# Performance work log

Measured on AMD Instinct MI355X. Metric: run time of the kernel, lower is better.

Reference implementation:

```python
import jax, jax.numpy as jnp
import numpy as np

B, N, L, D = 16, 8192, 512, 384  # batch, points, latents, model dim
FF = 4 * D  # feedforward inner dim (after GEGLU split)


def _ln(x, g, b, eps=1e-5):
    m = jnp.mean(x, axis=-1, keepdims=True)
    v = jnp.mean((x - m) ** 2, axis=-1, keepdims=True)
    return (x - m) * jax.lax.rsqrt(v + eps) * g + b


def setup_inputs() -> dict:
    key = jax.random.key(0)
    ks = jax.random.split(key, 16)
    s = 0.02
    def w(k, shape):
        return jax.random.normal(k, shape, jnp.float32) * s
    return {
        "x": jax.random.normal(ks[0], (B, N, 3), jnp.float32),
        # MLP: in(3)->D, D->D, D->D, D->D with ReLU between (eqx-style depth=3)
        "mlp_w0": w(ks[1], (3, D)), "mlp_b0": jnp.zeros((D,), jnp.float32),
        "mlp_w1": w(ks[2], (D, D)), "mlp_b1": jnp.zeros((D,), jnp.float32),
        "mlp_w2": w(ks[3], (D, D)), "mlp_b2": jnp.zeros((D,), jnp.float32),
        "mlp_w3": w(ks[4], (D, D)), "mlp_b3": jnp.zeros((D,), jnp.float32),
        "query": jax.random.normal(ks[5], (1, L, D), jnp.float32),
        "ln_q_g": jnp.ones((D,), jnp.float32), "ln_q_b": jnp.zeros((D,), jnp.float32),
        "ln_ctx_g": jnp.ones((D,), jnp.float32), "ln_ctx_b": jnp.zeros((D,), jnp.float32),
        "wq": w(ks[6], (D, D)),
        "wkv": w(ks[7], (D, 2 * D)),
        "wo": w(ks[8], (D, D)), "bo": jnp.zeros((D,), jnp.float32),
        "ln_ff_g": jnp.ones((D,), jnp.float32), "ln_ff_b": jnp.zeros((D,), jnp.float32),
        "ff_w1": w(ks[9], (D, 2 * FF)), "ff_b1": jnp.zeros((2 * FF,), jnp.float32),
        "ff_w2": w(ks[10], (FF, D)), "ff_b2": jnp.zeros((D,), jnp.float32),
    }


def reference(x, mlp_w0, mlp_b0, mlp_w1, mlp_b1, mlp_w2, mlp_b2, mlp_w3, mlp_b3,
              query, ln_q_g, ln_q_b, ln_ctx_g, ln_ctx_b, wq, wkv, wo, bo,
              ln_ff_g, ln_ff_b, ff_w1, ff_b1, ff_w2, ff_b2):
    # point MLP: 3 -> D
    h = jax.nn.relu(x @ mlp_w0 + mlp_b0)
    h = jax.nn.relu(h @ mlp_w1 + mlp_b1)
    h = jax.nn.relu(h @ mlp_w2 + mlp_b2)
    ctx = h @ mlp_w3 + mlp_b3                      # [B, N, D]

    lq = jnp.broadcast_to(query, (x.shape[0], L, D))  # learnable latents

    # PreNorm cross-attention (heads=1, dim_head=D)
    qn = _ln(lq, ln_q_g, ln_q_b)
    cn = _ln(ctx, ln_ctx_g, ln_ctx_b)
    q = qn @ wq                                    # [B, L, D]
    kv = cn @ wkv
    k, v = jnp.split(kv, 2, axis=-1)               # [B, N, D] each
    scale = D ** -0.5
    sim = jnp.einsum('bid,bjd->bij', q, k) * scale # [B, L, N]
    attn = jax.nn.softmax(sim, axis=-1)
    out = jnp.einsum('bij,bjd->bid', attn, v)      # [B, L, D]
    x1 = (out @ wo + bo) + lq                      # residual

    # PreNorm GEGLU feedforward
    f = _ln(x1, ln_ff_g, ln_ff_b)
    f = f @ ff_w1 + ff_b1                          # [B, L, 2*FF]
    a, g = jnp.split(f, 2, axis=-1)
    f = a * jax.nn.gelu(g, approximate=False)      # GEGLU (exact gelu, torch default)
    return (f @ ff_w2 + ff_b2) + x1                # [B, L, D]
```

## Files before the change

kernel.cpp:

```cpp
#include <hip/hip_runtime.h>
#include <math.h>


typedef unsigned short u16;
typedef unsigned int   u32;
typedef __bf16 bf16_t;
typedef bf16_t bf16x8 __attribute__((ext_vector_type(8)));
typedef float  floatx4 __attribute__((ext_vector_type(4)));

__device__ __forceinline__ float b2f(u16 v) {
    return __uint_as_float(((u32)v) << 16);
}
__device__ __forceinline__ u16 f2b(float f) {
    bf16_t h = (bf16_t)f;
    return __builtin_bit_cast(u16, h);
}
__device__ __forceinline__ void stb4(u16* p, float4 f) {
    uint2 v;
    v.x = (u32)f2b(f.x) | ((u32)f2b(f.y) << 16);
    v.y = (u32)f2b(f.z) | ((u32)f2b(f.w) << 16);
    *(uint2*)p = v;
}

__device__ __forceinline__ void gl2lds16(u16* lds, const u16* g) {
    __builtin_amdgcn_global_load_lds(
        (const __attribute__((address_space(1))) void*)g,
        (__attribute__((address_space(3))) void*)lds, 16, 0, 0);
}

__device__ __forceinline__ void xcd_remap(int& bx, int& by, int& bz) {
    int gx = gridDim.x, gy = gridDim.y, gz = gridDim.z;
    int nb = gx * gy * gz;
    int p = bx + gx * (by + gy * bz);
    if ((nb & 7) == 0) {
        int chunk = nb >> 3;
        p = (p & 7) * chunk + (p >> 3);
    }
    bx = p % gx;
    int t = p / gx;
    by = t % gy;
    bz = t / gy;
}

__device__ __forceinline__ void xcd_remap_yf(int& bx, int& by, int& bz) {
    int gx = gridDim.x, gy = gridDim.y, gz = gridDim.z;
    int nb = gx * gy * gz;
    int p = by + gy * (bx + gx * bz);
    if ((nb & 7) == 0) {
        int chunk = nb >> 3;
        p = (p & 7) * chunk + (p >> 3);
    }
    by = p % gy;
    int t = p / gy;
    bx = t % gx;
    bz = t / gx;
}

__global__ __launch_bounds__(256) void wconv_all(
    const float* __restrict__ w1, const float* __restrict__ w2,
    const float* __restrict__ w3, const float* __restrict__ wq,
    const float* __restrict__ wkv, const float* __restrict__ wo,
    const float* __restrict__ ffw1, const float* __restrict__ ffw2,
    u16* __restrict__ d1, u16* __restrict__ d2, u16* __restrict__ d3,
    u16* __restrict__ dq, u16* __restrict__ dо,
    u16* __restrict__ dffw1, u16* __restrict__ dffw2,
    u16* __restrict__ dwkd, u16* __restrict__ dwvd)
{
    int idx = blockIdx.x * 256 + threadIdx.x;
    if (idx >= 2801664) return;
    if (idx >= 2654208) {
        int local = idx - 2654208;
        int dd = local / 384, c = local - dd * 384;
        dwvd[local] = f2b(wkv[(long long)dd * 768 + 384 + c]);
        return;
    }
    if (idx >= 2506752) {
        int local = idx - 2506752;
        int e = local / 384, d = local - e * 384;
        dwkd[local] = f2b(wkv[(long long)e * 768 + d]);
        return;
    }
    const float* W; u16* WT; int Kd, Nd, local;
    if      (idx <  147456) { W=w1;   WT=d1;    Kd=384;  Nd=384;  local=idx; }
    else if (idx <  294912) { W=w2;   WT=d2;    Kd=384;  Nd=384;  local=idx-147456; }
    else if (idx <  442368) { W=w3;   WT=d3;    Kd=384;  Nd=384;  local=idx-294912; }
    else if (idx <  589824) { W=wq;   WT=dq;    Kd=384;  Nd=384;  local=idx-442368; }
    else if (idx <  737280) { W=wo;   WT=dо;    Kd=384;  Nd=384;  local=idx-589824; }
    else if (idx < 1916928) { W=ffw1; WT=dffw1; Kd=384;  Nd=3072; local=idx-737280; }
    else                    { W=ffw2; WT=dffw2; Kd=1536; Nd=384;  local=idx-1916928; }
    int n = local / Kd, k = local - n * Kd;
    WT[local] = f2b(W[(long long)k * Nd + n]);
}

__global__ __launch_bounds__(256) void layer0_kernel(
    const float* __restrict__ X, const float* __restrict__ W0,
    const float* __restrict__ B0, u16* __restrict__ H, int total4)
{
    int idx = blockIdx.x * 256 + threadIdx.x;
    if (idx >= total4) return;
    int e = idx * 4;
    int m = e / 384;
    int j = e - m * 384;
    float x0 = X[m * 3 + 0], x1 = X[m * 3 + 1], x2 = X[m * 3 + 2];
    float4 w0 = *(const float4*)(W0 + j);
    float4 w1 = *(const float4*)(W0 + 384 + j);
    float4 w2 = *(const float4*)(W0 + 768 + j);
    float4 bb = *(const float4*)(B0 + j);
    float4 v;
    v.x = fmaxf(bb.x + x0 * w0.x + x1 * w1.x + x2 * w2.x, 0.f);
    v.y = fmaxf(bb.y + x0 * w0.y + x1 * w1.y + x2 * w2.y, 0.f);
    v.z = fmaxf(bb.z + x0 * w0.z + x1 * w1.z + x2 * w2.z, 0.f);
    v.w = fmaxf(bb.w + x0 * w0.w + x1 * w1.w + x2 * w2.w, 0.f);
    stb4(H + e, v);
}

template<int IN_F32>
__global__ __launch_bounds__(256) void ln_kernel(
    const void* __restrict__ Xv, const float* __restrict__ g,
    const float* __restrict__ b, u16* __restrict__ Y, int rows)
{
    int w = threadIdx.x >> 6, lane = threadIdx.x & 63;
    int row = blockIdx.x * 4 + w;
    if (row >= rows) return;
    float v[6];
    float s = 0.f, ss = 0.f;
#pragma unroll
    for (int i = 0; i < 6; ++i) {
        int c = i * 64 + lane;
        v[i] = IN_F32 ? ((const float*)Xv)[(long long)row * 384 + c]
                      : b2f(((const u16*)Xv)[(long long)row * 384 + c]);
        s += v[i]; ss += v[i] * v[i];
    }
#pragma unroll
    for (int m = 32; m; m >>= 1) {
        s  += __shfl_xor(s, m, 64);
        ss += __shfl_xor(ss, m, 64);
    }
    float mean = s * (1.0f / 384.0f);
    float var  = ss * (1.0f / 384.0f) - mean * mean;
    float rs = rsqrtf(fmaxf(var, 0.f) + 1e-5f);
    u16* yr = Y + (long long)row * 384;
#pragma unroll
    for (int i = 0; i < 6; ++i) {
        int c = i * 64 + lane;
        yr[c] = f2b((v[i] - mean) * rs * g[c] + b[c]);
    }
}

__global__ __launch_bounds__(256) void ln_tr_kernel(
    const u16* __restrict__ Xv, const float* __restrict__ g,
    const float* __restrict__ b, u16* __restrict__ Y, u16* __restrict__ YT)
{
    __shared__ u16 tr[384 * 72];
    int w = threadIdx.x >> 6, lane = threadIdx.x & 63;
    int row0 = blockIdx.x * 64;
    for (int rr = 0; rr < 16; ++rr) {
        int jl = w * 16 + rr;
        long long row = row0 + jl;
        float v[6];
        float s = 0.f, ss = 0.f;
#pragma unroll
        for (int i = 0; i < 6; ++i) {
            int c = i * 64 + lane;
            v[i] = b2f(Xv[row * 384 + c]);
            s += v[i]; ss += v[i] * v[i];
        }
#pragma unroll
        for (int m = 32; m; m >>= 1) {
            s  += __shfl_xor(s, m, 64);
            ss += __shfl_xor(ss, m, 64);
        }
        float mean = s * (1.0f / 384.0f);
        float var  = ss * (1.0f / 384.0f) - mean * mean;
        float rs = rsqrtf(fmaxf(var, 0.f) + 1e-5f);
        u16* yr = Y + row * 384;
#pragma unroll
        for (int i = 0; i < 6; ++i) {
            int c = i * 64 + lane;
            u16 val = f2b((v[i] - mean) * rs * g[c] + b[c]);
            yr[c] = val;
            tr[c * 72 + jl] = val;
        }
    }
    __syncthreads();
    int gb = row0 >> 13;
    int jloc = row0 & 8191;
    u16* yt = YT + (long long)gb * 384 * 8192 + jloc;
    for (int e = threadIdx.x; e < 384; e += 256) {
        const u16* src = &tr[e * 72];
        u16* dst = yt + (long long)e * 8192;
#pragma unroll
        for (int q = 0; q < 8; ++q)
            *(uint4*)(dst + q * 8) = *(const uint4*)(src + q * 8);
    }
}

#define STAGE_AB3(bufi, kk)                                                    \
    { u16* asd_ = shmem + (bufi) * 4096;                                       \
      u16* bsd_ = shmem + 12288 + (bufi) * 4096;                               \
      gl2lds16(asd_ + (wv * 32) * 32,                                          \
          aptr_ + (long long)(m0 + wv * 32 + rlo_) * lda_ + (kk) + c8_);       \
      gl2lds16(asd_ + (wv * 32 + 16) * 32,                                     \
          aptr_ + (long long)(m0 + wv * 32 + 16 + rlo_) * lda_ + (kk) + c8_);  \
      gl2lds16(bsd_ + (wv * 32) * 32,                                          \
          bptr_ + (long long)(n0 + wv * 32 + rlo_) * ldb_ + (kk) + c8_);       \
      gl2lds16(bsd_ + (wv * 32 + 16) * 32,                                     \
          bptr_ + (long long)(n0 + wv * 32 + 16 + rlo_) * ldb_ + (kk) + c8_); }

#define MFMA_TILE_PIPE(Aptr, Bptr, LDA, LDB, K0, K1)                           \
    {                                                                          \
        const u16* aptr_ = (Aptr); const u16* bptr_ = (Bptr);                  \
        const long long lda_ = (LDA), ldb_ = (LDB);                            \
        const int rlo_ = lane >> 2, c8_ = (lane & 3) * 8;                      \
        const int T_ = ((K1) - (K0)) >> 5;                                     \
        STAGE_AB3(0, (K0))                                                     \
        STAGE_AB3(1, (K0) + 32)                                                \
        int cur = 0;                                                           \
        for (int t = 0; t < T_; ++t) {                                         \
            if (t + 1 < T_) { asm volatile("s_waitcnt vmcnt(4)" ::: "memory"); } \
            else            { asm volatile("s_waitcnt vmcnt(0)" ::: "memory"); } \
            __builtin_amdgcn_s_barrier();                                      \
            if (t + 2 < T_) {                                                  \
                int stg = (cur == 0) ? 2 : cur - 1;                            \
                STAGE_AB3(stg, (K0) + (t + 2) * 32)                            \
            }                                                                  \
            const u16* As_ = shmem + cur * 4096;                               \
            const u16* Bs_ = shmem + 12288 + cur * 4096;                       \
            bf16x8 a0 = *(const bf16x8*)&As_[(wv * 32 + lr) * 32 + lq * 8];    \
            bf16x8 a1 = *(const bf16x8*)&As_[(wv * 32 + 16 + lr) * 32 + lq * 8]; \
            _Pragma("unroll")                                                  \
            for (int ns = 0; ns < 8; ++ns) {                                   \
                bf16x8 b = *(const bf16x8*)&Bs_[(ns * 16 + lr) * 32 + lq * 8]; \
                acc[0][ns] = __builtin_amdgcn_mfma_f32_16x16x32_bf16(a0, b, acc[0][ns], 0, 0, 0); \
                acc[1][ns] = __builtin_amdgcn_mfma_f32_16x16x32_bf16(a1, b, acc[1][ns], 0, 0, 0); \
            }                                                                  \
            cur = (cur == 2) ? 0 : cur + 1;                                    \
        }                                                                      \
    }

#define STAGE_AB2(bufi, kk)                                                    \
    { u16* asd_ = shmem + (bufi) * 4096;                                       \
      u16* bsd_ = shmem + 8192 + (bufi) * 4096;                                \
      gl2lds16(asd_ + (wv * 32) * 32,                                          \
          aptr_ + (long long)(m0 + wv * 32 + rlo_) * lda_ + (kk) + c8_);       \
      gl2lds16(asd_ + (wv * 32 + 16) * 32,                                     \
          aptr_ + (long long)(m0 + wv * 32 + 16 + rlo_) * lda_ + (kk) + c8_);  \
      gl2lds16(bsd_ + (wv * 32) * 32,                                          \
          bptr_ + (long long)(n0 + wv * 32 + rlo_) * ldb_ + (kk) + c8_);       \
      gl2lds16(bsd_ + (wv * 32 + 16) * 32,                                     \
          bptr_ + (long long)(n0 + wv * 32 + 16 + rlo_) * ldb_ + (kk) + c8_); }

#define MFMA_TILE_DBUF(Aptr, Bptr, LDA, LDB, K0, K1)                           \
    {                                                                          \
        const u16* aptr_ = (Aptr); const u16* bptr_ = (Bptr);                  \
        const long long lda_ = (LDA), ldb_ = (LDB);                            \
        const int rlo_ = lane >> 2, c8_ = (lane & 3) * 8;                      \
        int cur = 0;                                                           \
        STAGE_AB2(0, (K0))                                                     \
        for (int k0 = (K0); k0 < (K1); k0 += 32) {                             \
            __syncthreads();                                                   \
            if (k0 + 32 < (K1)) STAGE_AB2(cur ^ 1, k0 + 32)                    \
            const u16* As_ = shmem + cur * 4096;                               \
            const u16* Bs_ = shmem + 8192 + cur * 4096;                        \
            bf16x8 a0 = *(const bf16x8*)&As_[(wv * 32 + lr) * 32 + lq * 8];    \
            bf16x8 a1 = *(const bf16x8*)&As_[(wv * 32 + 16 + lr) * 32 + lq * 8]; \
            _Pragma("unroll")                                                  \
            for (int ns = 0; ns < 8; ++ns) {                                   \
                bf16x8 b = *(const bf16x8*)&Bs_[(ns * 16 + lr) * 32 + lq * 8]; \
                acc[0][ns] = __builtin_amdgcn_mfma_f32_16x16x32_bf16(a0, b, acc[0][ns], 0, 0, 0); \
                acc[1][ns] = __builtin_amdgcn_mfma_f32_16x16x32_bf16(a1, b, acc[1][ns], 0, 0, 0); \
            }                                                                  \
            cur ^= 1;                                                          \
        }                                                                      \
    }

template<int RES_F32, int OUT_F32>
__global__ __launch_bounds__(256) void gemm_mfma(
    const u16* __restrict__ A, const u16* __restrict__ WT,
    const float* __restrict__ bias, const void* __restrict__ res,
    void* __restrict__ C,
    int M, int N, int K, int lda, int ldb, int ldc, int ldres,
    float scale, int relu, int resmask,
    long long zsA, long long zsB, long long zsC)
{
    __shared__ u16 shmem[24576];
    const int tid = threadIdx.x;
    const int wv = tid >> 6, lane = tid & 63;
    const int lr = lane & 15, lq = lane >> 4;
    int bx = blockIdx.x, by = blockIdx.y, bz = blockIdx.z;
    xcd_remap_yf(bx, by, bz);
    const int m0 = bx * 128;
    const int n0 = by * 128;
    const u16* Az = A + bz * zsA;
    const u16* Bz = WT + bz * zsB;
    const long long czoff = bz * zsC;

    floatx4 acc[2][8];
#pragma unroll
    for (int i = 0; i < 2; ++i)
#pragma unroll
        for (int j = 0; j < 8; ++j)
            acc[i][j] = (floatx4){0.f, 0.f, 0.f, 0.f};

    MFMA_TILE_PIPE(Az, Bz, lda, ldb, 0, K)

    float bi[8];
#pragma unroll
    for (int ns = 0; ns < 8; ++ns)
        bi[ns] = bias ? bias[n0 + ns * 16 + lr] : 0.f;

#pragma unroll
    for (int ms = 0; ms < 2; ++ms) {
#pragma unroll
        for (int r = 0; r < 4; ++r) {
            int m = m0 + wv * 32 + ms * 16 + lq * 4 + r;
#pragma unroll
            for (int ns = 0; ns < 8; ++ns) {
                int col = n0 + ns * 16 + lr;
                float v = acc[ms][ns][r] * scale + bi[ns];
                if (relu) v = fmaxf(v, 0.f);
                if (res) {
                    long long ro = (long long)(m & resmask) * ldres + col;
                    v += RES_F32 ? ((const float*)res)[ro]
                                 : b2f(((const u16*)res)[ro]);
                }
                long long co = czoff + (long long)m * ldc + col;
                if (OUT_F32) ((float*)C)[co] = v;
                else         ((u16*)C)[co] = f2b(v);
            }
        }
    }
}

__global__ __launch_bounds__(256) void gemm_exp(
    const u16* __restrict__ A, const u16* __restrict__ WT,
    u16* __restrict__ P, float* __restrict__ den,
    int K, int lda, int ldb, int ldc,
    long long zsB, long long zsP)
{
    __shared__ u16 shmem[16384];
    const int tid = threadIdx.x;
    const int wv = tid >> 6, lane = tid & 63;
    const int lr = lane & 15, lq = lane >> 4;
    int bx = blockIdx.x, by = blockIdx.y, bz = blockIdx.z;
    xcd_remap(bx, by, bz);
    const int m0 = bx * 128;
    const int n0 = by * 128;
    const u16* Bz = WT + bz * zsB;
    u16* Pz = P + bz * zsP;
    float* dz = den + bz * 512;

    floatx4 acc[2][8];
#pragma unroll
    for (int i = 0; i < 2; ++i)
#pragma unroll
        for (int j = 0; j < 8; ++j)
            acc[i][j] = (floatx4){0.f, 0.f, 0.f, 0.f};

    MFMA_TILE_DBUF(A, Bz, lda, ldb, 0, K)

    u16* sh = shmem;
    float srow[2][4] = {};
#pragma unroll
    for (int ms = 0; ms < 2; ++ms) {
        __syncthreads();
#pragma unroll
        for (int ns = 0; ns < 8; ++ns)
#pragma unroll
            for (int r = 0; r < 4; ++r) {
                float l = acc[ms][ns][r];
                l = fminf(fmaxf(l, -60.f), 60.f);
                float p = __expf(l);
                srow[ms][r] += p;
                int row = wv * 16 + lq * 4 + r;
                int col = (ns * 16 + lr) ^ (((row >> 3) & 1) << 3);
                sh[row * 136 + col] = f2b(p);
            }
        __syncthreads();
#pragma unroll
        for (int j = 0; j < 4; ++j) {
            int idx = j * 256 + tid;
            int rl = idx >> 4, ch = idx & 15;
            int m = m0 + ((rl >> 4) << 5) + ms * 16 + (rl & 15);
            int src = rl * 136 + ((ch * 8) ^ ((((rl >> 3) & 1)) << 3));
            *(uint4*)&Pz[(long long)m * ldc + n0 + ch * 8] =
                *(const uint4*)&sh[src];
        }
    }
#pragma unroll
    for (int ms = 0; ms < 2; ++ms)
#pragma unroll
        for (int r = 0; r < 4; ++r) {
            float s = srow[ms][r];
            s += __shfl_xor(s, 1, 64);
            s += __shfl_xor(s, 2, 64);
            s += __shfl_xor(s, 4, 64);
            s += __shfl_xor(s, 8, 64);
            if (lr == 0)
                atomicAdd(&dz[m0 + wv * 32 + ms * 16 + lq * 4 + r], s);
        }
}

__global__ __launch_bounds__(256) void gemm_pv(
    const u16* __restrict__ P, const u16* __restrict__ KT,
    const float* __restrict__ den, u16* __restrict__ part, int SPLIT)
{
    __shared__ u16 shmem[24576];
    const int tid = threadIdx.x;
    const int wv = tid >> 6, lane = tid & 63;
    const int lr = lane & 15, lq = lane >> 4;
    int bx = blockIdx.x, by = blockIdx.y, bz = blockIdx.z;
    xcd_remap(bx, by, bz);
    const int m0 = bx * 128;
    const int n0 = by * 128;
    const int g = bz / SPLIT, sp = bz - g * SPLIT;
    const int chunk = 8192 / SPLIT;
    const u16* Az = P + (long long)g * 512 * 8192;
    const u16* Bz = KT + (long long)g * 384 * 8192;
    const float* dg = den + g * 512;

    floatx4 acc[2][8];
#pragma unroll
    for (int i = 0; i < 2; ++i)
#pragma unroll
        for (int j = 0; j < 8; ++j)
            acc[i][j] = (floatx4){0.f, 0.f, 0.f, 0.f};

    MFMA_TILE_PIPE(Az, Bz, 8192, 8192, sp * chunk, sp * chunk + chunk)

    u16* pz = part + (long long)bz * 512 * 384;
#pragma unroll
    for (int ms = 0; ms < 2; ++ms)
#pragma unroll
        for (int r = 0; r < 4; ++r) {
            int m = m0 + wv * 32 + ms * 16 + lq * 4 + r;
            float inv = 1.0f / dg[m];
#pragma unroll
            for (int ns = 0; ns < 8; ++ns) {
                int col = n0 + ns * 16 + lr;
                pz[(long long)m * 384 + col] = f2b(acc[ms][ns][r] * inv);
            }
        }
}

__global__ __launch_bounds__(256) void pv_reduce_kernel(
    const u16* __restrict__ part, u16* __restrict__ AO, int SPLIT)
{
    int idx = blockIdx.x * 256 + threadIdx.x;
    int q = idx / 96, j = (idx - q * 96) * 4;
    int g = q >> 9, ql = q & 511;
    const u16* base = part + ((long long)g * SPLIT * 512 + ql) * 384 + j;
    float4 s = make_float4(0.f, 0.f, 0.f, 0.f);
    for (int sp = 0; sp < SPLIT; ++sp) {
        uint2 v = *(const uint2*)(base + (long long)sp * 512 * 384);
        s.x += b2f((u16)(v.x & 0xffff));
        s.y += b2f((u16)(v.x >> 16));
        s.z += b2f((u16)(v.y & 0xffff));
        s.w += b2f((u16)(v.y >> 16));
    }
    stb4(AO + (long long)q * 384 + j, s);
}

__global__ __launch_bounds__(256) void gemm_ff1_geglu(
    const u16* __restrict__ A, const u16* __restrict__ WT,
    const float* __restrict__ bias, u16* __restrict__ C,
    int K, int lda, int ldb, int ldc)
{
    __shared__ u16 shmem[24576];
    const int tid = threadIdx.x;
    const int wv = tid >> 6, lane = tid & 63;
    const int lr = lane & 15, lq = lane >> 4;
    int bx = blockIdx.x, by = blockIdx.y, bz = blockIdx.z;
    xcd_remap_yf(bx, by, bz);
    const int m0 = bx * 128;
    const int n0 = by * 64;
    const int rlo = lane >> 2, c8 = (lane & 3) * 8;

    floatx4 accA[2][4], accG[2][4];
#pragma unroll
    for (int i = 0; i < 2; ++i)
#pragma unroll
        for (int j = 0; j < 4; ++j) {
            accA[i][j] = (floatx4){0.f, 0.f, 0.f, 0.f};
            accG[i][j] = (floatx4){0.f, 0.f, 0.f, 0.f};
        }

#define STAGE_FF(bufi, kk)                                                     \
    { u16* asd = shmem + (bufi) * 4096;                                        \
      u16* bsd = shmem + 12288 + (bufi) * 4096;                                \
      gl2lds16(asd + (wv * 32) * 32,                                           \
          A + (long long)(m0 + wv * 32 + rlo) * lda + (kk) + c8);              \
      gl2lds16(asd + (wv * 32 + 16) * 32,                                      \
          A + (long long)(m0 + wv * 32 + 16 + rlo) * lda + (kk) + c8);         \
      int r0 = wv * 32 + rlo, r1 = r0 + 16;                                    \
      int wrow0 = (r0 < 64) ? (n0 + r0) : (1536 + n0 + r0 - 64);               \
      int wrow1 = (r1 < 64) ? (n0 + r1) : (1536 + n0 + r1 - 64);               \
      gl2lds16(bsd + (wv * 32) * 32, WT + (long long)wrow0 * ldb + (kk) + c8); \
      gl2lds16(bsd + (wv * 32 + 16) * 32, WT + (long long)wrow1 * ldb + (kk) + c8); }

    const int T = K >> 5;
    STAGE_FF(0, 0)
    STAGE_FF(1, 32)
    int cur = 0;
    for (int t = 0; t < T; ++t) {
        if (t + 1 < T) { asm volatile("s_waitcnt vmcnt(4)" ::: "memory"); }
        else           { asm volatile("s_waitcnt vmcnt(0)" ::: "memory"); }
        __builtin_amdgcn_s_barrier();
        if (t + 2 < T) {
            int stg = (cur == 0) ? 2 : cur - 1;
            STAGE_FF(stg, (t + 2) * 32)
        }
        const u16* As_ = shmem + cur * 4096;
        const u16* Bs_ = shmem + 12288 + cur * 4096;
        bf16x8 a0 = *(const bf16x8*)&As_[(wv * 32 + lr) * 32 + lq * 8];
        bf16x8 a1 = *(const bf16x8*)&As_[(wv * 32 + 16 + lr) * 32 + lq * 8];
#pragma unroll
        for (int ns = 0; ns < 4; ++ns) {
            bf16x8 bA = *(const bf16x8*)&Bs_[(ns * 16 + lr) * 32 + lq * 8];
            bf16x8 bG = *(const bf16x8*)&Bs_[((64 + ns * 16) + lr) * 32 + lq * 8];
            accA[0][ns] = __builtin_amdgcn_mfma_f32_16x16x32_bf16(a0, bA, accA[0][ns], 0, 0, 0);
            accA[1][ns] = __builtin_amdgcn_mfma_f32_16x16x32_bf16(a1, bA, accA[1][ns], 0, 0, 0);
            accG[0][ns] = __builtin_amdgcn_mfma_f32_16x16x32_bf16(a0, bG, accG[0][ns], 0, 0, 0);
            accG[1][ns] = __builtin_amdgcn_mfma_f32_16x16x32_bf16(a1, bG, accG[1][ns], 0, 0, 0);
        }
        cur = (cur == 2) ? 0 : cur + 1;
    }
#undef STAGE_FF

    float ba[4], bg[4];
#pragma unroll
    for (int ns = 0; ns < 4; ++ns) {
        ba[ns] = bias[n0 + ns * 16 + lr];
        bg[ns] = bias[1536 + n0 + ns * 16 + lr];
    }
#pragma unroll
    for (int ms = 0; ms < 2; ++ms)
#pragma unroll
        for (int r = 0; r < 4; ++r) {
            int m = m0 + wv * 32 + ms * 16 + lq * 4 + r;
#pragma unroll
            for (int ns = 0; ns < 4; ++ns) {
                int col = n0 + ns * 16 + lr;
                float a = accA[ms][ns][r] + ba[ns];
                float g = accG[ms][ns][r] + bg[ns];
                float v = a * 0.5f * g * (1.0f + erff(g * 0.70710678118654752f));
                C[(long long)m * ldc + col] = f2b(v);
            }
        }
}

extern "C" void kernel_launch(void* const* d_in, const int* in_sizes, int n_in,
                              void* d_out, int out_size, void* d_ws, size_t ws_size,
                              hipStream_t stream) {
    const float* x     = (const float*)d_in[0];
    const float* w0    = (const float*)d_in[1];
    const float* b0    = (const float*)d_in[2];
    const float* w1    = (const float*)d_in[3];
    const float* b1    = (const float*)d_in[4];
    const float* w2    = (const float*)d_in[5];
    const float* b2    = (const float*)d_in[6];
    const float* w3    = (const float*)d_in[7];
    const float* b3    = (const float*)d_in[8];
    const float* query = (const float*)d_in[9];
    const float* lnqg  = (const float*)d_in[10];
    const float* lnqb  = (const float*)d_in[11];
    const float* lncg  = (const float*)d_in[12];
    const float* lncb  = (const float*)d_in[13];
    const float* wq    = (const float*)d_in[14];
    const float* wkv   = (const float*)d_in[15];
    const float* wo    = (const float*)d_in[16];
    const float* bo    = (const float*)d_in[17];
    const float* lnfg  = (const float*)d_in[18];
    const float* lnfb  = (const float*)d_in[19];
    const float* ffw1  = (const float*)d_in[20];
    const float* ffb1  = (const float*)d_in[21];
    const float* ffw2  = (const float*)d_in[22];
    const float* ffb2  = (const float*)d_in[23];
    float* out = (float*)d_out;
    char* wsb = (char*)d_ws;

    auto need = [](int G) -> size_t {
        return (size_t)G * (3LL * 6291456 + 8388608)
             + 25165824
             + 6291456
             + 3 * 393216 + 32768
             + 5898240;
    };
    int G = 2;
    if      (ws_size >= need(16)) G = 16;
    else if (ws_size >= need(8))  G = 8;
    else if (ws_size >= need(4))  G = 4;
    const int SPLIT = 64 / G;

    long long off = 0;
    u16*   bufA   = (u16*)(wsb + off); off += (long long)G * 6291456;
    u16*   bufB   = (u16*)(wsb + off); off += (long long)G * 6291456;
    u16*   knT    = (u16*)(wsb + off); off += (long long)G * 6291456;
    u16*   Pb     = (u16*)(wsb + off); off += (long long)G * 8388608;
    u16*   part   = (u16*)(wsb + off); off += 25165824;
    u16*   ao_all = (u16*)(wsb + off); off += 6291456;
    u16*   qn     = (u16*)(wsb + off); off += 393216;
    u16*   qb     = (u16*)(wsb + off); off += 393216;
    u16*   q2     = (u16*)(wsb + off); off += 393216;
    float* den    = (float*)(wsb + off); off += 32768;
    u16*   w1T    = (u16*)(wsb + off); off += 294912;
    u16*   w2T    = (u16*)(wsb + off); off += 294912;
    u16*   w3T    = (u16*)(wsb + off); off += 294912;
    u16*   wqT    = (u16*)(wsb + off); off += 294912;
    u16*   woT    = (u16*)(wsb + off); off += 294912;
    u16*   ffw1T  = (u16*)(wsb + off); off += 2359296;
    u16*   ffw2T  = (u16*)(wsb + off); off += 1179648;
    u16*   wkdir  = (u16*)(wsb + off); off += 294912;
    u16*   wvdir  = (u16*)(wsb + off); off += 294912;
    u16*   wvoT   = (u16*)(wsb + off); off += 294912;
    u16*   x1_all = (u16*)(wsb + 0);
    u16*   f0_all = (u16*)(wsb + 6291456);
    u16*   gl_all = (u16*)(wsb + 12582912);

    const int FULLMASK = 0x3FFFFFFF;

    wconv_all<<<10944, 256, 0, stream>>>(w1, w2, w3, wq, wkv, wo, ffw1, ffw2,
        w1T, w2T, w3T, wqT, woT, ffw1T, ffw2T, wkdir, wvdir);
    hipMemsetAsync(den, 0, 16 * 512 * sizeof(float), stream);
    ln_kernel<1><<<128, 256, 0, stream>>>(query, lnqg, lnqb, qn, 512);
    gemm_mfma<0, 0><<<dim3(4, 3), 256, 0, stream>>>(qn, wqT, nullptr, nullptr, qb,
        512, 384, 384, 384, 384, 384, 0, 1.f, 0, FULLMASK, 0, 0, 0);
    gemm_mfma<0, 0><<<dim3(4, 3), 256, 0, stream>>>(qb, wkdir, nullptr, nullptr, q2,
        512, 384, 384, 384, 384, 384, 0, 0.05103103630798288f, 0, FULLMASK, 0, 0, 0);
    gemm_mfma<0, 0><<<dim3(3, 3), 256, 0, stream>>>(woT, wvdir, nullptr, nullptr, wvoT,
        384, 384, 384, 384, 384, 384, 0, 1.f, 0, FULLMASK, 0, 0, 0);

    const int MG = G * 8192;
    for (int base = 0; base < 16; base += G) {
        const float* xg = x + (long long)base * 24576;

        layer0_kernel<<<G * 3072, 256, 0, stream>>>(xg, w0, b0, bufA, G * 786432);
        gemm_mfma<0, 0><<<dim3(MG / 128, 3), 256, 0, stream>>>(bufA, w1T, b1, nullptr, bufB,
            MG, 384, 384, 384, 384, 384, 0, 1.f, 1, FULLMASK, 0, 0, 0);
        gemm_mfma<0, 0><<<dim3(MG / 128, 3), 256, 0, stream>>>(bufB, w2T, b2, nullptr, bufA,
            MG, 384, 384, 384, 384, 384, 0, 1.f, 1, FULLMASK, 0, 0, 0);
        gemm_mfma<0, 0><<<dim3(MG / 128, 3), 256, 0, stream>>>(bufA, w3T, b3, nullptr, bufB,
            MG, 384, 384, 384, 384, 384, 0, 1.f, 0, FULLMASK, 0, 0, 0);
        ln_tr_kernel<<<MG / 64, 256, 0, stream>>>(bufB, lncg, lncb, bufA, knT);
        gemm_exp<<<dim3(4, 64, G), 256, 0, stream>>>(q2, bufA, Pb, den + base * 512,
            384, 384, 384, 8192, 8192LL * 384, 512LL * 8192);
        gemm_pv<<<dim3(4, 3, G * SPLIT), 256, 0, stream>>>(Pb, knT, den + base * 512,
            part, SPLIT);
        pv_reduce_kernel<<<G * 192, 256, 0, stream>>>(part,
            ao_all + (long long)base * 196608, SPLIT);
    }

    gemm_mfma<1, 0><<<dim3(64, 3), 256, 0, stream>>>(ao_all, wvoT, bo, query, x1_all,
        8192, 384, 384, 384, 384, 384, 384, 1.f, 0, 511, 0, 0, 0);
    ln_kernel<0><<<2048, 256, 0, stream>>>(x1_all, lnfg, lnfb, f0_all, 8192);
    gemm_ff1_geglu<<<dim3(64, 24), 256, 0, stream>>>(f0_all, ffw1T, ffb1, gl_all,
        384, 384, 384, 1536);
    gemm_mfma<0, 1><<<dim3(64, 3), 256, 0, stream>>>(gl_all, ffw2T, ffb2, x1_all, out,
        8192, 384, 1536, 1536, 1536, 384, 384, 1.f, 0, FULLMASK, 0, 0, 0);
}
```

Baseline: 766.8 us.

## Fuse QK-exp and PV GEMMs into one attention kernel without materializing P

Replaces the separate gemm_exp (which wrote the exponentiated score matrix P to global memory) and gemm_pv kernels with a single attn_fused kernel. It computes exp scores per 128-key window into LDS and multiplies them directly by the staged V tiles, accumulating the output in registers. Normalization by the softmax denominator moves into pv_reduce. This removes the large P buffer write and read and drops a launch. In exchange it reloads Q tiles for every key window, uses 512-thread blocks with heavier register use, and caps the group size G at 8, which means more loop iterations.

```diff
diff --git a/kernel.cpp b/kernel.cpp
--- a/kernel.cpp
+++ b/kernel.cpp
@@ -238,42 +238,6 @@
         }                                                                      \
     }
 
-#define STAGE_AB2(bufi, kk)                                                    \
-    { u16* asd_ = shmem + (bufi) * 4096;                                       \
-      u16* bsd_ = shmem + 8192 + (bufi) * 4096;                                \
-      gl2lds16(asd_ + (wv * 32) * 32,                                          \
-          aptr_ + (long long)(m0 + wv * 32 + rlo_) * lda_ + (kk) + c8_);       \
-      gl2lds16(asd_ + (wv * 32 + 16) * 32,                                     \
-          aptr_ + (long long)(m0 + wv * 32 + 16 + rlo_) * lda_ + (kk) + c8_);  \
-      gl2lds16(bsd_ + (wv * 32) * 32,                                          \
-          bptr_ + (long long)(n0 + wv * 32 + rlo_) * ldb_ + (kk) + c8_);       \
-      gl2lds16(bsd_ + (wv * 32 + 16) * 32,                                     \
-          bptr_ + (long long)(n0 + wv * 32 + 16 + rlo_) * ldb_ + (kk) + c8_); }
-
-#define MFMA_TILE_DBUF(Aptr, Bptr, LDA, LDB, K0, K1)                           \
-    {                                                                          \
-        const u16* aptr_ = (Aptr); const u16* bptr_ = (Bptr);                  \
-        const long long lda_ = (LDA), ldb_ = (LDB);                            \
-        const int rlo_ = lane >> 2, c8_ = (lane & 3) * 8;                      \
-        int cur = 0;                                                           \
-        STAGE_AB2(0, (K0))                                                     \
-        for (int k0 = (K0); k0 < (K1); k0 += 32) {                             \
-            __syncthreads();                                                   \
-            if (k0 + 32 < (K1)) STAGE_AB2(cur ^ 1, k0 + 32)                    \
-            const u16* As_ = shmem + cur * 4096;                               \
-            const u16* Bs_ = shmem + 8192 + cur * 4096;                        \
-            bf16x8 a0 = *(const bf16x8*)&As_[(wv * 32 + lr) * 32 + lq * 8];    \
-            bf16x8 a1 = *(const bf16x8*)&As_[(wv * 32 + 16 + lr) * 32 + lq * 8]; \
-            _Pragma("unroll")                                                  \
-            for (int ns = 0; ns < 8; ++ns) {                                   \
-                bf16x8 b = *(const bf16x8*)&Bs_[(ns * 16 + lr) * 32 + lq * 8]; \
-                acc[0][ns] = __builtin_amdgcn_mfma_f32_16x16x32_bf16(a0, b, acc[0][ns], 0, 0, 0); \
-                acc[1][ns] = __builtin_amdgcn_mfma_f32_16x16x32_bf16(a1, b, acc[1][ns], 0, 0, 0); \
-            }                                                                  \
-            cur ^= 1;                                                          \
-        }                                                                      \
-    }
-
 template<int RES_F32, int OUT_F32>
 __global__ __launch_bounds__(256) void gemm_mfma(
     const u16* __restrict__ A, const u16* __restrict__ WT,
@@ -332,119 +296,129 @@
     }
 }
 
-__global__ __launch_bounds__(256) void gemm_exp(
-    const u16* __restrict__ A, const u16* __restrict__ WT,
-    u16* __restrict__ P, float* __restrict__ den,
-    int K, int lda, int ldb, int ldc,
-    long long zsB, long long zsP)
-{
-    __shared__ u16 shmem[16384];
+#define STAGE_QK(bi, kt)                                                       \
+    { int rw_ = tid >> 2, qt_ = tid & 3;                                       \
+      gl2lds16(QBs[bi] + tid * 8,                                              \
+          KN + (knbase + key0 + rw_) * 384 + (kt) * 32 + qt_ * 8);             \
+      if (tid < 256)                                                           \
+          gl2lds16(QAs[bi] + tid * 8,                                          \
+              Q2 + (long long)(q0 + rw_) * 384 + (kt) * 32 + qt_ * 8); }
+
+__global__ __launch_bounds__(512) void attn_fused(
+    const u16* __restrict__ Q2, const u16* __restrict__ KN,
+    const u16* __restrict__ KT, float* __restrict__ den,
+    u16* __restrict__ part, int SPLIT)
+{
+    __shared__ u16 shmem[32768];
+    u16* S = shmem;
+    u16* QAs[2] = { shmem + 8192,  shmem + 10240 };
+    u16* QBs[2] = { shmem + 12288, shmem + 16384 };
+    u16* PB = shmem + 20480;
+
     const int tid = threadIdx.x;
-    const int wv = tid >> 6, lane = tid & 63;
+    const int lane = tid & 63;
     const int lr = lane & 15, lq = lane >> 4;
-    int bx = blockIdx.x, by = blockIdx.y, bz = blockIdx.z;
-    xcd_remap(bx, by, bz);
-    const int m0 = bx * 128;
-    const int n0 = by * 128;
-    const u16* Bz = WT + bz * zsB;
-    u16* Pz = P + bz * zsP;
-    float* dz = den + bz * 512;
-
-    floatx4 acc[2][8];
-#pragma unroll
-    for (int i = 0; i < 2; ++i)
-#pragma unroll
-        for (int j = 0; j < 8; ++j)
-            acc[i][j] = (floatx4){0.f, 0.f, 0.f, 0.f};
-
-    MFMA_TILE_DBUF(A, Bz, lda, ldb, 0, K)
-
-    u16* sh = shmem;
-    float srow[2][4] = {};
-#pragma unroll
-    for (int ms = 0; ms < 2; ++ms) {
+    const int w8 = tid >> 6;
+    const int rg = w8 >> 1, half = w8 & 1;
+    int bx = blockIdx.x, by = blockIdx.y;
+    {
+        int nb = gridDim.x * gridDim.y;
+        int p = bx + gridDim.x * by;
+        if ((nb & 7) == 0) { int ch = nb >> 3; p = (p & 7) * ch + (p >> 3); }
+        bx = p % gridDim.x; by = p / gridDim.x;
+    }
+    const int q0 = bx * 64;
+    const int z = by;
+    const int g = z / SPLIT, sp = z - g * SPLIT;
+    const int chunk = 8192 / SPLIT;
+    const int windows = chunk >> 7;
+    const long long knbase = (long long)g * 8192;
+    const u16* KTg = KT + (long long)g * 384 * 8192;
+
+    floatx4 oacc[12];
+#pragma unroll
+    for (int i = 0; i < 12; ++i) oacc[i] = (floatx4){0.f, 0.f, 0.f, 0.f};
+    float denacc[4] = {0.f, 0.f, 0.f, 0.f};
+
+    for (int kw = 0; kw < windows; ++kw) {
+        const long long key0 = (long long)sp * chunk + kw * 128;
+
+        floatx4 sacc[4];
+#pragma unroll
+        for (int i = 0; i < 4; ++i) sacc[i] = (floatx4){0.f, 0.f, 0.f, 0.f};
+        STAGE_QK(0, 0)
+        int cur = 0;
+        for (int t = 0; t < 12; ++t) {
+            __syncthreads();
+            if (t + 1 < 12) STAGE_QK(cur ^ 1, t + 1)
+            bf16x8 a = *(const bf16x8*)&QAs[cur][(rg * 16 + lr) * 32 + lq * 8];
+#pragma unroll
+            for (int nt = 0; nt < 4; ++nt) {
+                bf16x8 b = *(const bf16x8*)&QBs[cur][(half * 64 + nt * 16 + lr) * 32 + lq * 8];
+                sacc[nt] = __builtin_amdgcn_mfma_f32_16x16x32_bf16(a, b, sacc[nt], 0, 0, 0);
+            }
+            cur ^= 1;
+        }
         __syncthreads();
 #pragma unroll
-        for (int ns = 0; ns < 8; ++ns)
+        for (int nt = 0; nt < 4; ++nt)
 #pragma unroll
             for (int r = 0; r < 4; ++r) {
-                float l = acc[ms][ns][r];
-                l = fminf(fmaxf(l, -60.f), 60.f);
+                float l = fminf(fmaxf(sacc[nt][r], -60.f), 60.f);
                 float p = __expf(l);
-                srow[ms][r] += p;
-                int row = wv * 16 + lq * 4 + r;
-                int col = (ns * 16 + lr) ^ (((row >> 3) & 1) << 3);
-                sh[row * 136 + col] = f2b(p);
+                int qrow = rg * 16 + lq * 4 + r;
+                int key = half * 64 + nt * 16 + lr;
+                int col = key ^ ((qrow & 7) << 3);
+                S[qrow * 128 + col] = f2b(p);
+                denacc[r] += p;
             }
         __syncthreads();
-#pragma unroll
-        for (int j = 0; j < 4; ++j) {
-            int idx = j * 256 + tid;
-            int rl = idx >> 4, ch = idx & 15;
-            int m = m0 + ((rl >> 4) << 5) + ms * 16 + (rl & 15);
-            int src = rl * 136 + ((ch * 8) ^ ((((rl >> 3) & 1)) << 3));
-            *(uint4*)&Pz[(long long)m * ldc + n0 + ch * 8] =
-                *(const uint4*)&sh[src];
-        }
-    }
-#pragma unroll
-    for (int ms = 0; ms < 2; ++ms)
-#pragma unroll
-        for (int r = 0; r < 4; ++r) {
-            float s = srow[ms][r];
-            s += __shfl_xor(s, 1, 64);
-            s += __shfl_xor(s, 2, 64);
-            s += __shfl_xor(s, 4, 64);
-            s += __shfl_xor(s, 8, 64);
-            if (lr == 0)
-                atomicAdd(&dz[m0 + wv * 32 + ms * 16 + lq * 4 + r], s);
-        }
-}
-
-__global__ __launch_bounds__(256) void gemm_pv(
-    const u16* __restrict__ P, const u16* __restrict__ KT,
-    const float* __restrict__ den, u16* __restrict__ part, int SPLIT)
-{
-    __shared__ u16 shmem[24576];
-    const int tid = threadIdx.x;
-    const int wv = tid >> 6, lane = tid & 63;
-    const int lr = lane & 15, lq = lane >> 4;
-    int bx = blockIdx.x, by = blockIdx.y, bz = blockIdx.z;
-    xcd_remap(bx, by, bz);
-    const int m0 = bx * 128;
-    const int n0 = by * 128;
-    const int g = bz / SPLIT, sp = bz - g * SPLIT;
-    const int chunk = 8192 / SPLIT;
-    const u16* Az = P + (long long)g * 512 * 8192;
-    const u16* Bz = KT + (long long)g * 384 * 8192;
-    const float* dg = den + g * 512;
-
-    floatx4 acc[2][8];
-#pragma unroll
-    for (int i = 0; i < 2; ++i)
-#pragma unroll
-        for (int j = 0; j < 8; ++j)
-            acc[i][j] = (floatx4){0.f, 0.f, 0.f, 0.f};
-
-    MFMA_TILE_PIPE(Az, Bz, 8192, 8192, sp * chunk, sp * chunk + chunk)
-
-    u16* pz = part + (long long)bz * 512 * 384;
-#pragma unroll
-    for (int ms = 0; ms < 2; ++ms)
-#pragma unroll
-        for (int r = 0; r < 4; ++r) {
-            int m = m0 + wv * 32 + ms * 16 + lq * 4 + r;
-            float inv = 1.0f / dg[m];
-#pragma unroll
-            for (int ns = 0; ns < 8; ++ns) {
-                int col = n0 + ns * 16 + lr;
-                pz[(long long)m * 384 + col] = f2b(acc[ms][ns][r] * inv);
+        for (int ks = 0; ks < 4; ++ks) {
+#pragma unroll
+            for (int i = 0; i < 3; ++i) {
+                int slot = i * 512 + tid;
+                int rw = slot >> 2, qt = slot & 3;
+                gl2lds16(PB + slot * 8,
+                    KTg + (long long)rw * 8192 + key0 + ks * 32 + qt * 8);
             }
-        }
+            __syncthreads();
+            int arow = rg * 16 + lr;
+            int acol = (ks * 32 + lq * 8) ^ ((arow & 7) << 3);
+            bf16x8 a = *(const bf16x8*)&S[arow * 128 + acol];
+#pragma unroll
+            for (int nt = 0; nt < 12; ++nt) {
+                bf16x8 b = *(const bf16x8*)&PB[(half * 192 + nt * 16 + lr) * 32 + lq * 8];
+                oacc[nt] = __builtin_amdgcn_mfma_f32_16x16x32_bf16(a, b, oacc[nt], 0, 0, 0);
+            }
+            __syncthreads();
+        }
+    }
+
+#pragma unroll
+    for (int r = 0; r < 4; ++r) {
+        float s = denacc[r];
+        s += __shfl_xor(s, 1, 64);
+        s += __shfl_xor(s, 2, 64);
+        s += __shfl_xor(s, 4, 64);
+        s += __shfl_xor(s, 8, 64);
+        if (lr == 0)
+            atomicAdd(&den[g * 512 + q0 + rg * 16 + lq * 4 + r], s);
+    }
+    u16* pz = part + (long long)z * 512 * 384;
+#pragma unroll
+    for (int r = 0; r < 4; ++r) {
+        int qrow = rg * 16 + lq * 4 + r;
+#pragma unroll
+        for (int nt = 0; nt < 12; ++nt) {
+            int d = half * 192 + nt * 16 + lr;
+            pz[(long long)(q0 + qrow) * 384 + d] = f2b(oacc[nt][r]);
+        }
+    }
 }
 
 __global__ __launch_bounds__(256) void pv_reduce_kernel(
-    const u16* __restrict__ part, u16* __restrict__ AO, int SPLIT)
+    const u16* __restrict__ part, const float* __restrict__ den,
+    u16* __restrict__ AO, int SPLIT)
 {
     int idx = blockIdx.x * 256 + threadIdx.x;
     int q = idx / 96, j = (idx - q * 96) * 4;
@@ -458,6 +432,8 @@
         s.z += b2f((u16)(v.y & 0xffff));
         s.w += b2f((u16)(v.y >> 16));
     }
+    float inv = 1.0f / den[q];
+    s.x *= inv; s.y *= inv; s.z *= inv; s.w *= inv;
     stb4(AO + (long long)q * 384 + j, s);
 }
 
@@ -580,23 +556,23 @@
     char* wsb = (char*)d_ws;
 
     auto need = [](int G) -> size_t {
-        return (size_t)G * (3LL * 6291456 + 8388608)
+        return (size_t)G * (3LL * 6291456)
              + 25165824
              + 6291456
              + 3 * 393216 + 32768
-             + 5898240;
+             + 6193152;
     };
     int G = 2;
     if      (ws_size >= need(16)) G = 16;
     else if (ws_size >= need(8))  G = 8;
     else if (ws_size >= need(4))  G = 4;
+    if (G > 8) G = 8;
     const int SPLIT = 64 / G;
 
     long long off = 0;
     u16*   bufA   = (u16*)(wsb + off); off += (long long)G * 6291456;
     u16*   bufB   = (u16*)(wsb + off); off += (long long)G * 6291456;
     u16*   knT    = (u16*)(wsb + off); off += (long long)G * 6291456;
-    u16*   Pb     = (u16*)(wsb + off); off += (long long)G * 8388608;
     u16*   part   = (u16*)(wsb + off); off += 25165824;
     u16*   ao_all = (u16*)(wsb + off); off += 6291456;
     u16*   qn     = (u16*)(wsb + off); off += 393216;
@@ -642,11 +618,9 @@
         gemm_mfma<0, 0><<<dim3(MG / 128, 3), 256, 0, stream>>>(bufA, w3T, b3, nullptr, bufB,
             MG, 384, 384, 384, 384, 384, 0, 1.f, 0, FULLMASK, 0, 0, 0);
         ln_tr_kernel<<<MG / 64, 256, 0, stream>>>(bufB, lncg, lncb, bufA, knT);
-        gemm_exp<<<dim3(4, 64, G), 256, 0, stream>>>(q2, bufA, Pb, den + base * 512,
-            384, 384, 384, 8192, 8192LL * 384, 512LL * 8192);
-        gemm_pv<<<dim3(4, 3, G * SPLIT), 256, 0, stream>>>(Pb, knT, den + base * 512,
-            part, SPLIT);
-        pv_reduce_kernel<<<G * 192, 256, 0, stream>>>(part,
+        attn_fused<<<dim3(8, 64), 512, 0, stream>>>(q2, bufA, knT,
+            den + base * 512, part, SPLIT);
+        pv_reduce_kernel<<<G * 192, 256, 0, stream>>>(part, den + base * 512,
             ao_all + (long long)base * 196608, SPLIT);
     }
 
```

New measurement: 858.9 us. 12.0% more time.
